# Kernel tuning notes

Measured on AMD Instinct MI355X. Metric: run time of the kernel, lower is better.

Reference implementation:

```python
import jax, jax.numpy as jnp
import numpy as np


def setup_inputs() -> dict:
    key = jax.random.key(0)
    ks = jax.random.split(key, 7)
    B, T, D, H, DK, S = 16, 1, 4096, 32, 128, 2048
    return {
        "x": jax.random.normal(ks[0], (B, T, D), dtype=jnp.float32),
        "k_cache": jax.random.normal(ks[1], (B, H, S, DK), dtype=jnp.float32),
        "v_cache": jax.random.normal(ks[2], (B, H, S, DK), dtype=jnp.float32),
        "Wq": jax.random.normal(ks[3], (D, D), dtype=jnp.float32) * (D ** -0.5),
        "Wk": jax.random.normal(ks[4], (D, D), dtype=jnp.float32) * (D ** -0.5),
        "Wv": jax.random.normal(ks[5], (D, D), dtype=jnp.float32) * (D ** -0.5),
        "Wo": jax.random.normal(ks[6], (D, D), dtype=jnp.float32) * (D ** -0.5),
        "start_pos": 2047,
    }


def reference(x, k_cache, v_cache, Wq, Wk, Wv, Wo, start_pos):
    B, T, D = x.shape
    H, DK = k_cache.shape[1], k_cache.shape[3]
    end_pos = start_pos + T

    # QKV projections (nn.Linear with bias=False: y = x @ W.T), split heads -> (B, H, T, DK)
    def proj(W):
        return (x @ W.T).reshape(B, T, H, DK).transpose(0, 2, 1, 3)

    q = proj(Wq)
    k_new = proj(Wk)
    v_new = proj(Wv)

    # Scatter new K/V into the pre-allocated cache at start_pos (static slice)
    k_cache = jax.lax.dynamic_update_slice(k_cache, k_new, (0, 0, start_pos, 0))
    v_cache = jax.lax.dynamic_update_slice(v_cache, v_new, (0, 0, start_pos, 0))

    # Gather cached K/V up to end_pos
    k_all = k_cache[:, :, :end_pos]  # (B, H, end_pos, DK)
    v_all = v_cache[:, :, :end_pos]

    # Scaled dot-product attention with causal mask over cache positions
    scores = jnp.einsum("bhtd,bhsd->bhts", q, k_all) / jnp.sqrt(jnp.float32(DK))
    pos_q = start_pos + jnp.arange(T)          # query absolute positions
    pos_k = jnp.arange(end_pos)                # key absolute positions
    mask = pos_k[None, :] <= pos_q[:, None]    # (T, end_pos)
    scores = jnp.where(mask[None, None], scores, jnp.float32(-1e30))
    attn = jax.nn.softmax(scores, axis=-1)
    out = jnp.einsum("bhts,bhsd->bhtd", attn, v_all)

    # Merge heads and output projection
    out = out.transpose(0, 2, 1, 3).reshape(B, T, D)
    return out @ Wo.T
```

## Files before the change

kernel.cpp:

```cpp
#include <hip/hip_runtime.h>
#include <math.h>

constexpr int B  = 16;
constexpr int H  = 32;
constexpr int S  = 2048;
constexpr int DK = 128;
constexpr int D  = 4096;
constexpr int BH = B * H;

constexpr int NSPLIT = 4;
constexpr int CHUNK  = S / NSPLIT;
constexpr int NREC   = NSPLIT * 4;
constexpr int REC    = 132;

__global__ __launch_bounds__(256) void proj_kernel(
    const float* __restrict__ X,
    const float* __restrict__ W0,
    const float* __restrict__ W1,
    const float* __restrict__ W2,
    float* __restrict__ Y0,
    float* __restrict__ Y1,
    float* __restrict__ Y2)
{
    const int lane = threadIdx.x & 63;
    const int wid  = threadIdx.x >> 6;
    const int c0   = (blockIdx.x * 4 + wid) * 4;
    const int wsel = c0 >> 12;
    const int n0   = c0 & (D - 1);

    const float* Wp = (wsel == 0) ? W0 : (wsel == 1) ? W1 : W2;
    float*       Yp = (wsel == 0) ? Y0 : (wsel == 1) ? Y1 : Y2;

    const float4* w0 = (const float4*)(Wp + (size_t)(n0 + 0) * D);
    const float4* w1 = (const float4*)(Wp + (size_t)(n0 + 1) * D);
    const float4* w2 = (const float4*)(Wp + (size_t)(n0 + 2) * D);
    const float4* w3 = (const float4*)(Wp + (size_t)(n0 + 3) * D);
    const float4* x4 = (const float4*)X;

    float acc[16][4];
    #pragma unroll
    for (int b = 0; b < 16; ++b) {
        acc[b][0] = 0.f; acc[b][1] = 0.f; acc[b][2] = 0.f; acc[b][3] = 0.f;
    }

    for (int chunk = 0; chunk < 16; ++chunk) {
        const int d4 = chunk * 64 + lane;
        const float4 wv0 = w0[d4];
        const float4 wv1 = w1[d4];
        const float4 wv2 = w2[d4];
        const float4 wv3 = w3[d4];
        #pragma unroll
        for (int b = 0; b < 16; ++b) {
            const float4 xv = x4[b * (D / 4) + d4];
            acc[b][0] += xv.x * wv0.x + xv.y * wv0.y + xv.z * wv0.z + xv.w * wv0.w;
            acc[b][1] += xv.x * wv1.x + xv.y * wv1.y + xv.z * wv1.z + xv.w * wv1.w;
            acc[b][2] += xv.x * wv2.x + xv.y * wv2.y + xv.z * wv2.z + xv.w * wv2.w;
            acc[b][3] += xv.x * wv3.x + xv.y * wv3.y + xv.z * wv3.z + xv.w * wv3.w;
        }
    }

    #pragma unroll
    for (int b = 0; b < 16; ++b) {
        #pragma unroll
        for (int i = 0; i < 4; ++i) {
            float v = acc[b][i];
            #pragma unroll
            for (int off = 32; off; off >>= 1) v += __shfl_xor(v, off, 64);
            acc[b][i] = v;
        }
    }

    float outv = 0.f;
    #pragma unroll
    for (int b = 0; b < 16; ++b) {
        #pragma unroll
        for (int i = 0; i < 4; ++i) {
            if ((lane >> 2) == b && (lane & 3) == i) outv = acc[b][i];
        }
    }
    const int ob = lane >> 2;
    const int oi = lane & 3;
    Yp[(size_t)ob * D + n0 + oi] = outv;
}

__global__ __launch_bounds__(256) void attn_kernel(
    const float* __restrict__ q,
    const float* __restrict__ k_cache,
    const float* __restrict__ v_cache,
    const float* __restrict__ k_new,
    const float* __restrict__ v_new,
    const int*   __restrict__ start_pos_p,
    float* __restrict__ part)
{
    const int lane  = threadIdx.x & 63;
    const int wid   = threadIdx.x >> 6;
    const int bh    = blockIdx.x & (BH - 1);
    const int split = blockIdx.x >> 9;

    const int sp      = start_pos_p[0];
    const int end_pos = sp + 1;

    const int s0    = split * CHUNK;
    int s_end = s0 + CHUNK;
    if (s_end > end_pos) s_end = end_pos;

    const float scale = 0.08838834764831845f;
    float2 qv = *(const float2*)(q + (size_t)bh * DK + 2 * lane);
    qv.x *= scale; qv.y *= scale;

    const float* kbase = k_cache + (size_t)bh * S * DK;
    const float* vbase = v_cache + (size_t)bh * S * DK;
    const float* knew  = k_new + (size_t)bh * DK;
    const float* vnew  = v_new + (size_t)bh * DK;

    float m = -INFINITY, l = 0.f, a0 = 0.f, a1 = 0.f;

    for (int s = s0 + wid; s < s_end; s += 4) {
        const bool is_new = (s == sp);
        const float* kp = is_new ? knew : (kbase + (size_t)s * DK);
        const float* vp = is_new ? vnew : (vbase + (size_t)s * DK);
        const float2 kv = *(const float2*)(kp + 2 * lane);
        const float2 vv = *(const float2*)(vp + 2 * lane);

        float p = kv.x * qv.x + kv.y * qv.y;
        #pragma unroll
        for (int off = 32; off; off >>= 1) p += __shfl_xor(p, off, 64);

        const float mn = fmaxf(m, p);
        const float eo = __expf(m - mn);
        const float ep = __expf(p - mn);
        l  = l  * eo + ep;
        a0 = a0 * eo + ep * vv.x;
        a1 = a1 * eo + ep * vv.y;
        m  = mn;
    }

    float* rec = part + ((size_t)bh * NREC + split * 4 + wid) * REC;
    *(float2*)(rec + 2 * lane) = make_float2(a0, a1);
    if (lane == 0) { rec[128] = m; rec[129] = l; }
}

__global__ __launch_bounds__(64) void combine_kernel(
    const float* __restrict__ part,
    float* __restrict__ attn_out)
{
    const int bh   = blockIdx.x;
    const int lane = threadIdx.x;
    const float* base = part + (size_t)bh * NREC * REC;

    float M = -INFINITY;
    #pragma unroll
    for (int i = 0; i < NREC; ++i) M = fmaxf(M, base[i * REC + 128]);

    float L = 0.f, o0 = 0.f, o1 = 0.f;
    #pragma unroll
    for (int i = 0; i < NREC; ++i) {
        const float mi = base[i * REC + 128];
        const float li = base[i * REC + 129];
        const float w  = __expf(mi - M);
        L += li * w;
        const float2 a = *(const float2*)(base + i * REC + 2 * lane);
        o0 += w * a.x;
        o1 += w * a.y;
    }
    const float inv = 1.f / L;
    attn_out[(size_t)bh * DK + 2 * lane]     = o0 * inv;
    attn_out[(size_t)bh * DK + 2 * lane + 1] = o1 * inv;
}

extern "C" void kernel_launch(void* const* d_in, const int* in_sizes, int n_in,
                              void* d_out, int out_size, void* d_ws, size_t ws_size,
                              hipStream_t stream)
{
    const float* x       = (const float*)d_in[0];
    const float* k_cache = (const float*)d_in[1];
    const float* v_cache = (const float*)d_in[2];
    const float* Wq      = (const float*)d_in[3];
    const float* Wk      = (const float*)d_in[4];
    const float* Wv      = (const float*)d_in[5];
    const float* Wo      = (const float*)d_in[6];
    const int*   sp      = (const int*)d_in[7];
    float*       out     = (float*)d_out;

    float* ws       = (float*)d_ws;
    float* q        = ws;
    float* k_new    = ws + 65536;
    float* v_new    = ws + 131072;
    float* attn_out = ws + 196608;
    float* part     = ws + 262144;

    proj_kernel<<<(3 * D) / 16, 256, 0, stream>>>(x, Wq, Wk, Wv, q, k_new, v_new);

    attn_kernel<<<BH * NSPLIT, 256, 0, stream>>>(q, k_cache, v_cache, k_new, v_new,
                                                 sp, part);

    combine_kernel<<<BH, 64, 0, stream>>>(part, attn_out);

    proj_kernel<<<D / 16, 256, 0, stream>>>(attn_out, Wo, Wo, Wo, out, out, out);
}
```

Baseline: 349.5 us.

## Stage x in LDS, split Wo K-dim across waves, float4 half-wave attention

The QKV projection now stages x tiles in double-buffered shared memory, prefetches the next weight and x chunk, and replaces 64 separate butterfly reductions with a transpose-style reduce64. The Wo projection gets its own kernel that splits the K dimension across the four waves, launching 1024 blocks instead of 256 to put more parallelism on the weight stream. Attention processes two cache positions per wave with float4 loads on half-waves and merges the halves before writing partials. The changes aim to make the weight and KV streaming more bandwidth-efficient, at the cost of more registers and LDS use.

```diff
diff --git a/kernel.cpp b/kernel.cpp
--- a/kernel.cpp
+++ b/kernel.cpp
@@ -13,7 +13,23 @@
 constexpr int NREC   = NSPLIT * 4;
 constexpr int REC    = 132;
 
-__global__ __launch_bounds__(256) void proj_kernel(
+__device__ __forceinline__ float reduce64(float v[64], int lane) {
+    #pragma unroll
+    for (int s = 0; s < 6; ++s) {
+        const int off = 1 << s;
+        #pragma unroll
+        for (int j = 0; j < (64 >> (s + 1)); ++j) {
+            const float lo = v[2 * j], hi = v[2 * j + 1];
+            const bool  up = (lane & off) != 0;
+            const float mine = up ? hi : lo;
+            const float oth  = up ? lo : hi;
+            v[j] = mine + __shfl_xor(oth, off, 64);
+        }
+    }
+    return v[0];
+}
+
+__global__ __launch_bounds__(256, 3) void proj_qkv_kernel(
     const float* __restrict__ X,
     const float* __restrict__ W0,
     const float* __restrict__ W1,
@@ -22,65 +38,109 @@
     float* __restrict__ Y1,
     float* __restrict__ Y2)
 {
+    __shared__ float4 xs[2][16][64];
+
+    const int t    = threadIdx.x;
+    const int lane = t & 63;
+    const int wid  = t >> 6;
+    const int tb   = t >> 4;
+    const int tf   = t & 15;
+
+    const int c0   = blockIdx.x * 16 + wid * 4;
+    const int wsel = c0 >> 12;
+    const int n0   = c0 & (D - 1);
+
+    const float* Wp = (wsel == 0) ? W0 : (wsel == 1) ? W1 : W2;
+    float*       Yp = (wsel == 0) ? Y0 : (wsel == 1) ? Y1 : Y2;
+    const float4* w4 = (const float4*)Wp;
+    const float4* x4 = (const float4*)X;
+
+    float acc[64];
+    #pragma unroll
+    for (int i = 0; i < 64; ++i) acc[i] = 0.f;
+
+    float4 xr[4];
+    #pragma unroll
+    for (int i = 0; i < 4; ++i) xr[i] = x4[tb * 1024 + tf + 16 * i];
+    float4 wv[4];
+    #pragma unroll
+    for (int c = 0; c < 4; ++c) wv[c] = w4[(size_t)(n0 + c) * 1024 + lane];
+    #pragma unroll
+    for (int i = 0; i < 4; ++i) xs[0][tb][tf + 16 * i] = xr[i];
+    __syncthreads();
+
+    for (int ch = 0; ch < 16; ++ch) {
+        float4 xn[4], wn[4];
+        const bool more = (ch < 15);
+        if (more) {
+            #pragma unroll
+            for (int i = 0; i < 4; ++i)
+                xn[i] = x4[tb * 1024 + (ch + 1) * 64 + tf + 16 * i];
+            #pragma unroll
+            for (int c = 0; c < 4; ++c)
+                wn[c] = w4[(size_t)(n0 + c) * 1024 + (ch + 1) * 64 + lane];
+        }
+        const int buf = ch & 1;
+        #pragma unroll
+        for (int b = 0; b < 16; ++b) {
+            const float4 xv = xs[buf][b][lane];
+            #pragma unroll
+            for (int c = 0; c < 4; ++c)
+                acc[b * 4 + c] += xv.x * wv[c].x + xv.y * wv[c].y +
+                                  xv.z * wv[c].z + xv.w * wv[c].w;
+        }
+        if (more) {
+            #pragma unroll
+            for (int i = 0; i < 4; ++i) xs[buf ^ 1][tb][tf + 16 * i] = xn[i];
+            __syncthreads();
+            #pragma unroll
+            for (int c = 0; c < 4; ++c) wv[c] = wn[c];
+        }
+    }
+
+    const float outv = reduce64(acc, lane);
+    Yp[(size_t)(lane >> 2) * D + n0 + (lane & 3)] = outv;
+}
+
+__global__ __launch_bounds__(256) void proj_wo_kernel(
+    const float* __restrict__ X,
+    const float* __restrict__ Wo,
+    float* __restrict__ out)
+{
+    __shared__ float red[4][64];
     const int lane = threadIdx.x & 63;
     const int wid  = threadIdx.x >> 6;
-    const int c0   = (blockIdx.x * 4 + wid) * 4;
-    const int wsel = c0 >> 12;
-    const int n0   = c0 & (D - 1);
-
-    const float* Wp = (wsel == 0) ? W0 : (wsel == 1) ? W1 : W2;
-    float*       Yp = (wsel == 0) ? Y0 : (wsel == 1) ? Y1 : Y2;
-
-    const float4* w0 = (const float4*)(Wp + (size_t)(n0 + 0) * D);
-    const float4* w1 = (const float4*)(Wp + (size_t)(n0 + 1) * D);
-    const float4* w2 = (const float4*)(Wp + (size_t)(n0 + 2) * D);
-    const float4* w3 = (const float4*)(Wp + (size_t)(n0 + 3) * D);
+    const int n0   = blockIdx.x * 4;
+    const float4* w4 = (const float4*)Wo;
     const float4* x4 = (const float4*)X;
 
-    float acc[16][4];
-    #pragma unroll
-    for (int b = 0; b < 16; ++b) {
-        acc[b][0] = 0.f; acc[b][1] = 0.f; acc[b][2] = 0.f; acc[b][3] = 0.f;
-    }
-
-    for (int chunk = 0; chunk < 16; ++chunk) {
-        const int d4 = chunk * 64 + lane;
-        const float4 wv0 = w0[d4];
-        const float4 wv1 = w1[d4];
-        const float4 wv2 = w2[d4];
-        const float4 wv3 = w3[d4];
+    float acc[64];
+    #pragma unroll
+    for (int i = 0; i < 64; ++i) acc[i] = 0.f;
+
+    #pragma unroll
+    for (int it = 0; it < 4; ++it) {
+        const int d4 = wid * 256 + it * 64 + lane;
+        float4 wv[4];
+        #pragma unroll
+        for (int c = 0; c < 4; ++c) wv[c] = w4[(size_t)(n0 + c) * 1024 + d4];
         #pragma unroll
         for (int b = 0; b < 16; ++b) {
-            const float4 xv = x4[b * (D / 4) + d4];
-            acc[b][0] += xv.x * wv0.x + xv.y * wv0.y + xv.z * wv0.z + xv.w * wv0.w;
-            acc[b][1] += xv.x * wv1.x + xv.y * wv1.y + xv.z * wv1.z + xv.w * wv1.w;
-            acc[b][2] += xv.x * wv2.x + xv.y * wv2.y + xv.z * wv2.z + xv.w * wv2.w;
-            acc[b][3] += xv.x * wv3.x + xv.y * wv3.y + xv.z * wv3.z + xv.w * wv3.w;
-        }
-    }
-
-    #pragma unroll
-    for (int b = 0; b < 16; ++b) {
-        #pragma unroll
-        for (int i = 0; i < 4; ++i) {
-            float v = acc[b][i];
-            #pragma unroll
-            for (int off = 32; off; off >>= 1) v += __shfl_xor(v, off, 64);
-            acc[b][i] = v;
-        }
-    }
-
-    float outv = 0.f;
-    #pragma unroll
-    for (int b = 0; b < 16; ++b) {
-        #pragma unroll
-        for (int i = 0; i < 4; ++i) {
-            if ((lane >> 2) == b && (lane & 3) == i) outv = acc[b][i];
-        }
-    }
-    const int ob = lane >> 2;
-    const int oi = lane & 3;
-    Yp[(size_t)ob * D + n0 + oi] = outv;
+            const float4 xv = x4[b * 1024 + d4];
+            #pragma unroll
+            for (int c = 0; c < 4; ++c)
+                acc[b * 4 + c] += xv.x * wv[c].x + xv.y * wv[c].y +
+                                  xv.z * wv[c].z + xv.w * wv[c].w;
+        }
+    }
+
+    const float pv = reduce64(acc, lane);
+    red[wid][lane] = pv;
+    __syncthreads();
+    if (wid == 0) {
+        const float tot = red[0][lane] + red[1][lane] + red[2][lane] + red[3][lane];
+        out[(size_t)(lane >> 2) * D + n0 + (lane & 3)] = tot;
+    }
 }
 
 __global__ __launch_bounds__(256) void attn_kernel(
@@ -94,50 +154,70 @@
 {
     const int lane  = threadIdx.x & 63;
     const int wid   = threadIdx.x >> 6;
+    const int half  = lane >> 5;
+    const int hl    = lane & 31;
     const int bh    = blockIdx.x & (BH - 1);
     const int split = blockIdx.x >> 9;
 
-    const int sp      = start_pos_p[0];
-    const int end_pos = sp + 1;
-
+    const int sp    = start_pos_p[0];
     const int s0    = split * CHUNK;
-    int s_end = s0 + CHUNK;
-    if (s_end > end_pos) s_end = end_pos;
+    const int lim   = sp + 1;
+    const int s_end = (s0 + CHUNK < lim) ? (s0 + CHUNK) : lim;
 
     const float scale = 0.08838834764831845f;
-    float2 qv = *(const float2*)(q + (size_t)bh * DK + 2 * lane);
-    qv.x *= scale; qv.y *= scale;
+    float4 qv = *(const float4*)(q + (size_t)bh * DK + 4 * hl);
+    qv.x *= scale; qv.y *= scale; qv.z *= scale; qv.w *= scale;
 
     const float* kbase = k_cache + (size_t)bh * S * DK;
     const float* vbase = v_cache + (size_t)bh * S * DK;
     const float* knew  = k_new + (size_t)bh * DK;
     const float* vnew  = v_new + (size_t)bh * DK;
 
-    float m = -INFINITY, l = 0.f, a0 = 0.f, a1 = 0.f;
-
-    for (int s = s0 + wid; s < s_end; s += 4) {
-        const bool is_new = (s == sp);
-        const float* kp = is_new ? knew : (kbase + (size_t)s * DK);
-        const float* vp = is_new ? vnew : (vbase + (size_t)s * DK);
-        const float2 kv = *(const float2*)(kp + 2 * lane);
-        const float2 vv = *(const float2*)(vp + 2 * lane);
-
-        float p = kv.x * qv.x + kv.y * qv.y;
-        #pragma unroll
-        for (int off = 32; off; off >>= 1) p += __shfl_xor(p, off, 64);
+    float  m = -1e30f, l = 0.f;
+    float4 acc = make_float4(0.f, 0.f, 0.f, 0.f);
+
+    for (int s2 = s0 + 2 * wid; s2 < s_end; s2 += 8) {
+        const int  pos   = s2 + half;
+        const bool valid = pos < s_end;
+        const int  cpos  = valid ? pos : (s_end - 1);
+        const float* kp = (cpos == sp) ? knew : (kbase + (size_t)cpos * DK);
+        const float* vp = (cpos == sp) ? vnew : (vbase + (size_t)cpos * DK);
+        const float4 kv = *(const float4*)(kp + 4 * hl);
+        const float4 vv = *(const float4*)(vp + 4 * hl);
+
+        float p = kv.x * qv.x + kv.y * qv.y + kv.z * qv.z + kv.w * qv.w;
+        p += __shfl_xor(p, 1, 64);
+        p += __shfl_xor(p, 2, 64);
+        p += __shfl_xor(p, 4, 64);
+        p += __shfl_xor(p, 8, 64);
+        p += __shfl_xor(p, 16, 64);
+        p = valid ? p : -2e30f;
 
         const float mn = fmaxf(m, p);
         const float eo = __expf(m - mn);
         const float ep = __expf(p - mn);
-        l  = l  * eo + ep;
-        a0 = a0 * eo + ep * vv.x;
-        a1 = a1 * eo + ep * vv.y;
-        m  = mn;
-    }
+        l     = l     * eo + ep;
+        acc.x = acc.x * eo + ep * vv.x;
+        acc.y = acc.y * eo + ep * vv.y;
+        acc.z = acc.z * eo + ep * vv.z;
+        acc.w = acc.w * eo + ep * vv.w;
+        m = mn;
+    }
+
+    const float m2 = __shfl_xor(m, 32, 64);
+    const float M  = fmaxf(m, m2);
+    const float w  = __expf(m - M);
+    l *= w;
+    acc.x *= w; acc.y *= w; acc.z *= w; acc.w *= w;
+    l     += __shfl_xor(l, 32, 64);
+    acc.x += __shfl_xor(acc.x, 32, 64);
+    acc.y += __shfl_xor(acc.y, 32, 64);
+    acc.z += __shfl_xor(acc.z, 32, 64);
+    acc.w += __shfl_xor(acc.w, 32, 64);
 
     float* rec = part + ((size_t)bh * NREC + split * 4 + wid) * REC;
-    *(float2*)(rec + 2 * lane) = make_float2(a0, a1);
-    if (lane == 0) { rec[128] = m; rec[129] = l; }
+    if (half == 0) *(float4*)(rec + 4 * hl) = acc;
+    if (lane == 0) { rec[128] = M; rec[129] = l; }
 }
 
 __global__ __launch_bounds__(64) void combine_kernel(
@@ -148,7 +228,7 @@
     const int lane = threadIdx.x;
     const float* base = part + (size_t)bh * NREC * REC;
 
-    float M = -INFINITY;
+    float M = -1e30f;
     #pragma unroll
     for (int i = 0; i < NREC; ++i) M = fmaxf(M, base[i * REC + 128]);
 
@@ -189,12 +269,12 @@
     float* attn_out = ws + 196608;
     float* part     = ws + 262144;
 
-    proj_kernel<<<(3 * D) / 16, 256, 0, stream>>>(x, Wq, Wk, Wv, q, k_new, v_new);
+    proj_qkv_kernel<<<(3 * D) / 16, 256, 0, stream>>>(x, Wq, Wk, Wv, q, k_new, v_new);
 
     attn_kernel<<<BH * NSPLIT, 256, 0, stream>>>(q, k_cache, v_cache, k_new, v_new,
                                                  sp, part);
 
     combine_kernel<<<BH, 64, 0, stream>>>(part, attn_out);
 
-    proj_kernel<<<D / 16, 256, 0, stream>>>(attn_out, Wo, Wo, Wo, out, out, out);
-}
+    proj_wo_kernel<<<D / 4, 256, 0, stream>>>(attn_out, Wo, out);
+}
```

Result: faster. 306.9 us (-12.2%).
